# Performance work log

Measured on AMD Instinct MI355X. Metric: run time of the kernel, lower is better.

Reference implementation:

```python
import jax, jax.numpy as jnp
import numpy as np

BIT_W = 8   # config.bit_wt
BIT_A = 8   # config.bit_act (activations sliced 2 bits at a time)
STRIDE = (1, 1)
PAD = 1


def _conv(a, w):
    # NCHW input, OIHW weight, stride 1, symmetric padding 1 (matches wrapped Conv2d)
    return jax.lax.conv_general_dilated(
        a, w, window_strides=STRIDE, padding=[(PAD, PAD), (PAD, PAD)],
        dimension_numbers=("NCHW", "OIHW", "NCHW"))


def setup_inputs() -> dict:
    key = jax.random.key(0)
    k1, k2, k3 = jax.random.split(key, 3)
    x = jax.random.normal(k1, (64, 64, 56, 56), dtype=jnp.float32)
    weight = jax.random.normal(k2, (64, 64, 3, 3), dtype=jnp.float32)
    bias = jax.random.normal(k3, (64,), dtype=jnp.float32)
    scale_a = jnp.full((1,), 20.0, dtype=jnp.float32)      # conv_q.scale
    scale_w = jnp.full((1,), 20.0, dtype=jnp.float32)      # wrapped_module.weight_scale
    zero_point = jnp.full((1,), -128.0, dtype=jnp.float32)  # conv_q.zero_point
    return {"x": x, "weight": weight, "bias": bias,
            "scale_a": scale_a, "scale_w": scale_w, "zero_point": zero_point}


def reference(x, weight, bias, scale_a, scale_w, zero_point):
    sa = scale_a[0]
    sw = scale_w[0]
    zp = zero_point[0]
    # activation quantization: round(x*scale_a - zero_point), clamp to [0, 2^bit_act - 1]
    q_in = jnp.clip(jnp.round(x * sa - zp), 0.0, 2.0 ** BIT_A - 1.0)
    # weight quantization: round(w * scale_w), interpreted in two's complement
    q_w = jnp.round(weight * sw)
    w_off = q_w + 2.0 ** BIT_W  # (w + (1 << bit_weight)) before bit masking

    acc = jnp.zeros((), dtype=jnp.float32)
    for ba in range(BIT_A // 2):
        # 2-bit activation slice: (a >> 2*ba) & 3
        a_sl = jnp.mod(jnp.floor(q_in / (4.0 ** ba)), 4.0)
        for bw in range(BIT_W):
            # weight bit bw: ((w + 2^B) >> bw) & 1
            w_bit = jnp.mod(jnp.floor(w_off / (2.0 ** bw)), 2.0)
            r = _conv(a_sl, w_bit)
            sgn = -1.0 if bw == BIT_W - 1 else 1.0  # MSB = sign bit (two's complement)
            acc = acc + sgn * (2.0 ** (2 * ba + bw)) * r

    # zero-point correction: conv(ones * zp, q_w) added back (no-op when zp == 0)
    acc = acc + zp * _conv(jnp.ones_like(q_in), q_w)

    out = acc / (sw * sa) + bias[None, :, None, None]
    return out
```

## Files before the change

### kernel.cpp

```cpp
#include <hip/hip_runtime.h>


typedef int v4i __attribute__((ext_vector_type(4)));
typedef float v4f __attribute__((ext_vector_type(4)));

#define ROWB 80

__global__ __launch_bounds__(64) void prep_wq(const float* __restrict__ wt,
                                              const float* __restrict__ sw_p,
                                              const float* __restrict__ zp_p,
                                              signed char* __restrict__ w8,
                                              float* __restrict__ corr_tab) {
  const int o = blockIdx.x;
  const int i = threadIdx.x;
  const float sw = sw_p[0];
  const float* wp = wt + (size_t)(o * 64 + i) * 9;
  int q[9];
#pragma unroll
  for (int k = 0; k < 9; ++k) q[k] = (int)rintf(wp[k] * sw);
#pragma unroll
  for (int k = 0; k < 9; ++k)
    w8[(o * 9 + k) * 64 + i] = (signed char)(q[k] & 255);

  int stc[9], srw[9];
#pragma unroll
  for (int k = 0; k < 9; ++k) {
    int a = (int)(signed char)(q[k] & 255);
    int b = q[k];
#pragma unroll
    for (int off = 32; off; off >>= 1) {
      a += __shfl_xor(a, off);
      b += __shfl_xor(b, off);
    }
    stc[k] = a; srw[k] = b;
  }
  const float zp = zp_p[0];
  if (i < 9) {
    const int v = i / 3, hc = i % 3;
    float corr = 0.0f;
#pragma unroll
    for (int k = 0; k < 9; ++k) {
      const int kh = k / 3, kw = k % 3;
      const bool drop = (v == 1 && kh == 0) || (v == 2 && kh == 2) ||
                        (hc == 1 && kw == 0) || (hc == 2 && kw == 2);
      if (!drop) corr += 128.0f * (float)stc[k] + zp * (float)srw[k];
    }
    corr_tab[i * 64 + o] = corr;
  }
}

__global__ __launch_bounds__(256, 4) void conv_fused(
    const float* __restrict__ x, const signed char* __restrict__ w8,
    const float* __restrict__ corr_tab, const float* __restrict__ bias,
    const float* __restrict__ sa_p, const float* __restrict__ sw_p,
    const float* __restrict__ zp_p, float* __restrict__ out) {
  __shared__ __align__(16) signed char lds[6 * 58 * ROWB];
  const int tid = threadIdx.x;
  const int b = blockIdx.x;
  const int g = (b & 7) * 112 + (b >> 3);
  const int n = (g * 2341) >> 15;
  const int h0 = (g - n * 14) * 4;
  const float sa = sa_p[0], zp = zp_p[0];
  const float* xim = x + (size_t)n * 200704;

#pragma unroll 3
  for (int it = 0; it < 6; ++it) {
    const int idx = tid + 256 * it;
    if (idx < 1344) {
      const int cg = idx & 15;
      const int rem = idx >> 4;
      const int row = (rem * 2341) >> 15;
      const int w4 = rem - row * 14;
      const int ih = h0 - 1 + row;
      const bool valid = (unsigned)ih < 56u;
      int* const dst = (int*)lds + (row * 58 + w4 * 4 + 1) * (ROWB / 4) + cg;
      if (valid) {
        v4f v[4];
#pragma unroll
        for (int j = 0; j < 4; ++j)
          v[j] = *(const v4f*)(xim + (size_t)(cg * 4 + j) * 3136 + ih * 56 + w4 * 4);
#pragma unroll
        for (int e = 0; e < 4; ++e) {
          float qf[4];
#pragma unroll
          for (int j = 0; j < 4; ++j) {
            float tq;
            {
#pragma clang fp contract(off)
              tq = v[j][e] * sa - zp;
            }
            qf[j] = rintf(tq);
          }
          unsigned dw;
          asm("v_cvt_pk_u8_f32 %0, %1, 0, %2" : "=v"(dw) : "v"(qf[0]), "v"(0u));
          asm("v_cvt_pk_u8_f32 %0, %1, 1, %2" : "=v"(dw) : "v"(qf[1]), "v"(dw));
          asm("v_cvt_pk_u8_f32 %0, %1, 2, %2" : "=v"(dw) : "v"(qf[2]), "v"(dw));
          asm("v_cvt_pk_u8_f32 %0, %1, 3, %2" : "=v"(dw) : "v"(qf[3]), "v"(dw));
          dst[e * (ROWB / 4)] = (int)(dw ^ 0x80808080u);
        }
      } else {
#pragma unroll
        for (int e = 0; e < 4; ++e) dst[e * (ROWB / 4)] = 0;
      }
    } else {
      const int z = idx - 1344;
      const int loc = z >> 4, d = z & 15;
      const int row = loc >> 1, side = loc & 1;
      ((int*)lds)[(row * 58 + side * 57) * (ROWB / 4) + d] = 0;
    }
  }
  __syncthreads();

  const int lane = tid & 63;
  const int wv = tid >> 6;
  const int phalf = wv & 1;
  const int ogp = wv >> 1;
  const int ln = lane & 15;
  const int kg = lane >> 4;
  const int oa = ogp * 32 + ln;

  const signed char* wba = w8 + (size_t)oa * 576 + kg * 16;
  v4i Ba[9], Bb[9];
#pragma unroll
  for (int t = 0; t < 9; ++t) {
    Ba[t] = *(const v4i*)(wba + t * 64);
    Bb[t] = *(const v4i*)(wba + 9216 + t * 64);
  }

  const float sw = sw_p[0];
  const float rden = 1.0f / (sw * sa);
  const float boa = bias[oa], bob = bias[oa + 16];
  const float cFa = corr_tab[oa];
  const float cFb = corr_tab[oa + 16];
  float* const outa = out + (size_t)(n * 64 + oa) * 3136 + h0 * 56;
  float* const outb = outa + 16 * 3136;

#pragma unroll 1
  for (int t = 0; t < 7; ++t) {
    const int pb = phalf * 112 + t * 16;
    const int pa = pb + ln;
    const int hr = (pa * 9363) >> 19;
    const int wc = pa - hr * 56;
    const signed char* ab = lds + (hr * 58 + wc) * ROWB + kg * 16;
    v4i acca = {0, 0, 0, 0}, accb = {0, 0, 0, 0};
#pragma unroll
    for (int kh = 0; kh < 3; ++kh) {
#pragma unroll
      for (int kw = 0; kw < 3; ++kw) {
        const v4i A = *(const v4i*)(ab + (kh * 58 + kw) * ROWB);
        acca = __builtin_amdgcn_mfma_i32_16x16x64_i8(A, Ba[kh * 3 + kw], acca, 0, 0, 0);
        accb = __builtin_amdgcn_mfma_i32_16x16x64_i8(A, Bb[kh * 3 + kw], accb, 0, 0, 0);
      }
    }
    const int pxb = pb + kg * 4;
    float ta[4], tb[4];
#pragma unroll
    for (int e = 0; e < 4; ++e) {
      const int px = pxb + e;
      const int hh = (px * 9363) >> 19;
      const int ww = px - hh * 56;
      const int hg = h0 + hh;
      float ca = cFa, cb = cFb;
      if ((hg == 0) | (hg == 55) | (ww == 0) | (ww == 55)) {
        const int vcase = (hg == 0) ? 1 : ((hg == 55) ? 2 : 0);
        const int hcase = (ww == 0) ? 1 : ((ww == 55) ? 2 : 0);
        const int cidx = (vcase * 3 + hcase) * 64;
        ca = corr_tab[cidx + oa];
        cb = corr_tab[cidx + oa + 16];
      }
      ta[e] = ((float)acca[e] + ca) * rden + boa;
      tb[e] = ((float)accb[e] + cb) * rden + bob;
    }
    const v4f va = {ta[0], ta[1], ta[2], ta[3]};
    const v4f vb = {tb[0], tb[1], tb[2], tb[3]};
    __builtin_nontemporal_store(va, (v4f*)(outa + pxb));
    __builtin_nontemporal_store(vb, (v4f*)(outb + pxb));
  }
}

extern "C" void kernel_launch(void* const* d_in, const int* in_sizes, int n_in,
                              void* d_out, int out_size, void* d_ws, size_t ws_size,
                              hipStream_t stream) {
  const float* x    = (const float*)d_in[0];
  const float* wt   = (const float*)d_in[1];
  const float* bias = (const float*)d_in[2];
  const float* sa   = (const float*)d_in[3];
  const float* sw   = (const float*)d_in[4];
  const float* zp   = (const float*)d_in[5];
  float* out = (float*)d_out;

  char* ws = (char*)d_ws;
  signed char* w8 = (signed char*)ws;
  float* corr_tab = (float*)(ws + 36864);

  prep_wq<<<64, 64, 0, stream>>>(wt, sw, zp, w8, corr_tab);
  conv_fused<<<896, 256, 0, stream>>>(x, w8, corr_tab, bias, sa, sw, zp, out);
}
```

Baseline: 136.6 us.

## Replace padded LDS rows with XOR-swizzled 64-byte layout and plain output stores

The padded 80-byte-per-column LDS layout becomes a dense 64-byte layout. The 16-byte channel chunk is XOR-swizzled by column bits, so the MFMA A-fragment reads and the staging writes avoid bank conflicts while using less LDS. The inline v_cvt_pk_u8 packing is replaced by clamp, subtract and shift packing in plain C, and nontemporal output stores become regular float4 stores. It also lowers the staging loop unroll from 3 to 2. The extra packing ALU and the change in store cache behaviour could offset the LDS gains.

```diff
diff --git a/kernel.cpp b/kernel.cpp
--- a/kernel.cpp
+++ b/kernel.cpp
@@ -3,8 +3,6 @@
 
 typedef int v4i __attribute__((ext_vector_type(4)));
 typedef float v4f __attribute__((ext_vector_type(4)));
-
-#define ROWB 80
 
 __global__ __launch_bounds__(64) void prep_wq(const float* __restrict__ wt,
                                               const float* __restrict__ sw_p,
@@ -54,7 +52,7 @@
     const float* __restrict__ corr_tab, const float* __restrict__ bias,
     const float* __restrict__ sa_p, const float* __restrict__ sw_p,
     const float* __restrict__ zp_p, float* __restrict__ out) {
-  __shared__ __align__(16) signed char lds[6 * 58 * ROWB];
+  __shared__ __align__(16) signed char lds[22272];
   const int tid = threadIdx.x;
   const int b = blockIdx.x;
   const int g = (b & 7) * 112 + (b >> 3);
@@ -63,7 +61,7 @@
   const float sa = sa_p[0], zp = zp_p[0];
   const float* xim = x + (size_t)n * 200704;
 
-#pragma unroll 3
+#pragma unroll 2
   for (int it = 0; it < 6; ++it) {
     const int idx = tid + 256 * it;
     if (idx < 1344) {
@@ -73,15 +71,16 @@
       const int w4 = rem - row * 14;
       const int ih = h0 - 1 + row;
       const bool valid = (unsigned)ih < 56u;
-      int* const dst = (int*)lds + (row * 58 + w4 * 4 + 1) * (ROWB / 4) + cg;
+      v4f v[4];
       if (valid) {
-        v4f v[4];
 #pragma unroll
         for (int j = 0; j < 4; ++j)
           v[j] = *(const v4f*)(xim + (size_t)(cg * 4 + j) * 3136 + ih * 56 + w4 * 4);
+      }
 #pragma unroll
-        for (int e = 0; e < 4; ++e) {
-          float qf[4];
+      for (int e = 0; e < 4; ++e) {
+        int dw = 0;
+        if (valid) {
 #pragma unroll
           for (int j = 0; j < 4; ++j) {
             float tq;
@@ -89,24 +88,21 @@
 #pragma clang fp contract(off)
               tq = v[j][e] * sa - zp;
             }
-            qf[j] = rintf(tq);
+            float qf = rintf(tq);
+            qf = fminf(fmaxf(qf, 0.0f), 255.0f);
+            const int bb = ((int)qf - 128) & 255;
+            dw |= bb << (8 * j);
           }
-          unsigned dw;
-          asm("v_cvt_pk_u8_f32 %0, %1, 0, %2" : "=v"(dw) : "v"(qf[0]), "v"(0u));
-          asm("v_cvt_pk_u8_f32 %0, %1, 1, %2" : "=v"(dw) : "v"(qf[1]), "v"(dw));
-          asm("v_cvt_pk_u8_f32 %0, %1, 2, %2" : "=v"(dw) : "v"(qf[2]), "v"(dw));
-          asm("v_cvt_pk_u8_f32 %0, %1, 3, %2" : "=v"(dw) : "v"(qf[3]), "v"(dw));
-          dst[e * (ROWB / 4)] = (int)(dw ^ 0x80808080u);
         }
-      } else {
-#pragma unroll
-        for (int e = 0; e < 4; ++e) dst[e * (ROWB / 4)] = 0;
+        const int c = w4 * 4 + 1 + e;
+        const int t = (c >> 1) & 3;
+        ((int*)lds)[(row * 58 + c) * 16 + (((cg >> 2) ^ t) << 2) + (cg & 3)] = dw;
       }
     } else {
       const int z = idx - 1344;
       const int loc = z >> 4, d = z & 15;
       const int row = loc >> 1, side = loc & 1;
-      ((int*)lds)[(row * 58 + side * 57) * (ROWB / 4) + d] = 0;
+      ((int*)lds)[(row * 58 + side * 57) * 16 + d] = 0;
     }
   }
   __syncthreads();
@@ -141,13 +137,19 @@
     const int pa = pb + ln;
     const int hr = (pa * 9363) >> 19;
     const int wc = pa - hr * 56;
-    const signed char* ab = lds + (hr * 58 + wc) * ROWB + kg * 16;
+    int coff[3];
+#pragma unroll
+    for (int kw = 0; kw < 3; ++kw) {
+      const int c = wc + kw;
+      coff[kw] = c * 64 + ((kg ^ ((c >> 1) & 3)) << 4);
+    }
+    const signed char* rowb = lds + hr * 3712;
     v4i acca = {0, 0, 0, 0}, accb = {0, 0, 0, 0};
 #pragma unroll
     for (int kh = 0; kh < 3; ++kh) {
 #pragma unroll
       for (int kw = 0; kw < 3; ++kw) {
-        const v4i A = *(const v4i*)(ab + (kh * 58 + kw) * ROWB);
+        const v4i A = *(const v4i*)(rowb + kh * 3712 + coff[kw]);
         acca = __builtin_amdgcn_mfma_i32_16x16x64_i8(A, Ba[kh * 3 + kw], acca, 0, 0, 0);
         accb = __builtin_amdgcn_mfma_i32_16x16x64_i8(A, Bb[kh * 3 + kw], accb, 0, 0, 0);
       }
@@ -171,10 +173,8 @@
       ta[e] = ((float)acca[e] + ca) * rden + boa;
       tb[e] = ((float)accb[e] + cb) * rden + bob;
     }
-    const v4f va = {ta[0], ta[1], ta[2], ta[3]};
-    const v4f vb = {tb[0], tb[1], tb[2], tb[3]};
-    __builtin_nontemporal_store(va, (v4f*)(outa + pxb));
-    __builtin_nontemporal_store(vb, (v4f*)(outb + pxb));
+    *(float4*)(outa + pxb) = make_float4(ta[0], ta[1], ta[2], ta[3]);
+    *(float4*)(outb + pxb) = make_float4(tb[0], tb[1], tb[2], tb[3]);
   }
 }
 
```

Result: faster. 131.4 us (-3.9%).
